# Optimization experiments

Measured on AMD Instinct MI355X. Metric: run time of the kernel, lower is better.

The kernel has to match this reference:

```python
import jax, jax.numpy as jnp
import numpy as np


def setup_inputs() -> dict:
    key = jax.random.key(0)
    k1, k2, k3, k4, k5 = jax.random.split(key, 5)
    B, TQ, TK, DQ, DV, U = 4, 512, 512, 512, 512, 256
    query = jax.random.normal(k1, (B, TQ, DQ), dtype=jnp.float32)
    value = jax.random.normal(k2, (B, TK, DV), dtype=jnp.float32)
    W1 = jax.random.normal(k3, (DQ, U), dtype=jnp.float32) * (1.0 / np.sqrt(DQ))
    W2 = jax.random.normal(k4, (DV, U), dtype=jnp.float32) * (1.0 / np.sqrt(DV))
    scale = jax.random.normal(k5, (U,), dtype=jnp.float32)
    return {"query": query, "value": value, "W1": W1, "W2": W2, "scale": scale}


def reference(query, value, W1, W2, scale):
    # Dense projections (no bias)
    q = jnp.einsum('bqd,du->bqu', query, W1)   # [B, Tq, U]
    k = jnp.einsum('bkd,du->bku', value, W2)   # [B, Tk, U]
    # Keras AdditiveAttention (use_scale=True):
    # scores[b,q,k] = sum_u scale[u] * tanh(q[b,q,u] + k[b,k,u])
    t = jnp.tanh(q[:, :, None, :] + k[:, None, :, :])  # [B, Tq, Tk, U]
    scores = jnp.einsum('bqku,u->bqk', t, scale)        # [B, Tq, Tk]
    attention_weights = jax.nn.softmax(scores, axis=-1)
    return attention_weights
```

## Files before the change

kernel.cpp:

```cpp
#include <hip/hip_runtime.h>

#define BB 4
#define TQ 512
#define TK 512
#define DQ 512
#define UU 256
#define CSC 2.8853900817779268f
#define L2E 1.4426950408889634f
#define RQ 4

typedef unsigned short u16;
typedef unsigned int u32;
typedef short bf16x8 __attribute__((ext_vector_type(8)));
typedef float f32x4 __attribute__((ext_vector_type(4)));

__device__ __forceinline__ float fexp2(float x) { return __builtin_amdgcn_exp2f(x); }
__device__ __forceinline__ float frcp(float x)  { return __builtin_amdgcn_rcpf(x); }
__device__ __forceinline__ u32 pkhi(u32 a, u32 b) { return (b & 0xffff0000u) | (a >> 16); }

__global__ __launch_bounds__(256) void wsplit(
    const float* __restrict__ W1, const float* __restrict__ W2,
    u16* __restrict__ W1h, u16* __restrict__ W1l,
    u16* __restrict__ W2h, u16* __restrict__ W2l)
{
    __shared__ float tile[32][33];
    const int blk = blockIdx.x, t = threadIdx.x;
    const float* W = (blk >> 7) ? W2 : W1;
    u16* oh = (blk >> 7) ? W2h : W1h;
    u16* ol = (blk >> 7) ? W2l : W1l;
    const int tl = blk & 127;
    const int k0 = (tl >> 3) * 32, n0 = (tl & 7) * 32;
    const int kl = t >> 5, nl = t & 31;
    #pragma unroll
    for (int r = 0; r < 4; r++)
        tile[kl + 8 * r][nl] = W[(size_t)(k0 + kl + 8 * r) * UU + n0 + nl];
    __syncthreads();
    const int nr = t >> 5, kc = t & 31;
    #pragma unroll
    for (int r = 0; r < 4; r++) {
        const float v = tile[kc][nr + 8 * r];
        const u32 x = __float_as_uint(v);
        const u16 h = (u16)(x >> 16);
        const u16 l = (u16)(__float_as_uint(v - __uint_as_float(x & 0xffff0000u)) >> 16);
        oh[(size_t)(n0 + nr + 8 * r) * DQ + k0 + kc] = h;
        ol[(size_t)(n0 + nr + 8 * r) * DQ + k0 + kc] = l;
    }
}

__global__ __launch_bounds__(256) void proj3(
    const float* __restrict__ Aq, const float* __restrict__ Av,
    const u16* __restrict__ W1h, const u16* __restrict__ W1l,
    const u16* __restrict__ W2h, const u16* __restrict__ W2l,
    float* __restrict__ Eq, float* __restrict__ Ek)
{
    __shared__ __align__(16) char raw[10240];
    float* fin = (float*)raw;

    const int z = blockIdx.z;
    const float* A = z ? Av : Aq;
    const u16* Wh = z ? W2h : W1h;
    const u16* Wl = z ? W2l : W1l;

    const int t = threadIdx.x;
    const int m0 = blockIdx.x * 32, n0 = blockIdx.y * 64;
    const int wave = t >> 6, ln = t & 15, qd = (t & 63) >> 4;
    const int arow = t >> 3, ak4 = (t & 7) * 4;
    const int ncol = n0 + wave * 16 + ln;
    const u16* whp = Wh + (size_t)ncol * DQ + qd * 8;
    const u16* wlp = Wl + (size_t)ncol * DQ + qd * 8;

    f32x4 acc[2] = {};

    float4 a4 = *(const float4*)&A[(size_t)(m0 + arow) * DQ + ak4];
    bf16x8 whc = *(const bf16x8*)&whp[0];
    bf16x8 wlc = *(const bf16x8*)&wlp[0];

    for (int i = 0; i < DQ / 32; i++) {
        char* buf = raw + (i & 1) * 5120;
        u16* Ah_s = (u16*)buf;
        u16* Al_s = (u16*)(buf + 2560);
        {
            const float f[4] = {a4.x, a4.y, a4.z, a4.w};
            u32 x[4], lx[4];
            #pragma unroll
            for (int e = 0; e < 4; e++) {
                x[e]  = __float_as_uint(f[e]);
                lx[e] = __float_as_uint(f[e] - __uint_as_float(x[e] & 0xffff0000u));
            }
            uint2 hw, lw;
            hw.x = pkhi(x[0], x[1]);  hw.y = pkhi(x[2], x[3]);
            lw.x = pkhi(lx[0], lx[1]); lw.y = pkhi(lx[2], lx[3]);
            *(uint2*)&Ah_s[arow * 40 + ak4] = hw;
            *(uint2*)&Al_s[arow * 40 + ak4] = lw;
        }
        if (i + 1 < DQ / 32)
            a4 = *(const float4*)&A[(size_t)(m0 + arow) * DQ + (i + 1) * 32 + ak4];
        __syncthreads();

        bf16x8 whn, wln;
        if (i + 1 < DQ / 32) {
            whn = *(const bf16x8*)&whp[(i + 1) * 32];
            wln = *(const bf16x8*)&wlp[(i + 1) * 32];
        }

        bf16x8 ah[2], al[2];
        #pragma unroll
        for (int ii = 0; ii < 2; ii++) {
            const int ar = (ii * 16 + ln) * 40 + qd * 8;
            ah[ii] = *(const bf16x8*)&Ah_s[ar];
            al[ii] = *(const bf16x8*)&Al_s[ar];
        }
        #pragma unroll
        for (int ii = 0; ii < 2; ii++) {
            acc[ii] = __builtin_amdgcn_mfma_f32_16x16x32_bf16(ah[ii], whc, acc[ii], 0, 0, 0);
            acc[ii] = __builtin_amdgcn_mfma_f32_16x16x32_bf16(ah[ii], wlc, acc[ii], 0, 0, 0);
            acc[ii] = __builtin_amdgcn_mfma_f32_16x16x32_bf16(al[ii], whc, acc[ii], 0, 0, 0);
        }
        whc = whn; wlc = wln;
    }

    if (z == 0) {
        #pragma unroll
        for (int ii = 0; ii < 2; ii++) {
            #pragma unroll
            for (int r = 0; r < 4; r++) {
                const int m = m0 + ii * 16 + qd * 4 + r;
                Eq[(size_t)m * UU + ncol] = fexp2(CSC * acc[ii][r]);
            }
        }
    } else {
        __syncthreads();
        #pragma unroll
        for (int ii = 0; ii < 2; ii++) {
            #pragma unroll
            for (int r = 0; r < 4; r++) {
                const int ml = ii * 16 + qd * 4 + r;
                const int nl = wave * 16 + ln;
                fin[ml * 68 + nl] = fexp2(CSC * acc[ii][r]);
            }
        }
        __syncthreads();
        const int b = m0 >> 9, j0 = m0 & 511;
        #pragma unroll
        for (int p = 0; p < 2; p++) {
            const int idx = p * 256 + t;
            const int jl = idx & 31, u4 = idx >> 5;
            const float4 v = *(const float4*)&fin[jl * 68 + u4 * 4];
            ((float4*)Ek)[(size_t)(b * (UU / 4) + (n0 >> 2) + u4) * TK + j0 + jl] = v;
        }
    }
}

__global__ __launch_bounds__(512) void attn_softmax(
    const float* __restrict__ Eq,
    const float* __restrict__ Ek,
    const float* __restrict__ scale,
    float* __restrict__ out)
{
    __shared__ float redbuf[RQ][8];
    const int t  = threadIdx.x;
    const int b  = blockIdx.x >> 7;
    const int q0 = (blockIdx.x & 127) * RQ;
    const float*  qrow = Eq + (size_t)(b * TQ + q0) * UU;
    const float4* kb4  = (const float4*)Ek + (size_t)b * (UU / 4) * TK + t;

    float acc[RQ] = {};

    auto body = [&](const float4& kv, int g) {
        const float4 sc4 = *(const float4*)&scale[4 * g];
        const float* sf = (const float*)&sc4;
        const float* kf = (const float*)&kv;
        #pragma unroll
        for (int r = 0; r < RQ; r++) {
            const float4 q4 = *(const float4*)&qrow[(size_t)r * UU + 4 * g];
            const float* qf = (const float*)&q4;
            #pragma unroll
            for (int p = 0; p < 4; p += 2) {
                const float d0 = fmaf(qf[p],     kf[p],     1.0f);
                const float d1 = fmaf(qf[p + 1], kf[p + 1], 1.0f);
                const float num = fmaf(sf[p], d1, sf[p + 1] * d0);
                acc[r] = fmaf(num, frcp(d0 * d1), acc[r]);
            }
        }
    };

    float4 c0 = kb4[0];
    float4 c1 = kb4[(size_t)TK];
    float4 c2 = kb4[(size_t)2 * TK];
    float4 c3 = kb4[(size_t)3 * TK];
    for (int g = 0; g < UU / 4; g += 4) {
        float4 n0v, n1v, n2v, n3v;
        if (g + 4 < UU / 4) {
            n0v = kb4[(size_t)(g + 4) * TK];
            n1v = kb4[(size_t)(g + 5) * TK];
            n2v = kb4[(size_t)(g + 6) * TK];
            n3v = kb4[(size_t)(g + 7) * TK];
        }
        body(c0, g); body(c1, g + 1); body(c2, g + 2); body(c3, g + 3);
        c0 = n0v; c1 = n1v; c2 = n2v; c3 = n3v;
    }
    #pragma unroll
    for (int r = 0; r < RQ; r++) acc[r] *= -2.0f;

    const int wave = t >> 6, lane = t & 63;
    float m[RQ], p[RQ];

    #pragma unroll
    for (int r = 0; r < RQ; r++) {
        float v = acc[r];
        #pragma unroll
        for (int o = 32; o > 0; o >>= 1) v = fmaxf(v, __shfl_xor(v, o));
        if (lane == 0) redbuf[r][wave] = v;
    }
    __syncthreads();
    #pragma unroll
    for (int r = 0; r < RQ; r++) {
        float v = redbuf[r][0];
        #pragma unroll
        for (int w = 1; w < 8; w++) v = fmaxf(v, redbuf[r][w]);
        m[r] = v;
    }
    __syncthreads();

    #pragma unroll
    for (int r = 0; r < RQ; r++) {
        p[r] = fexp2(L2E * (acc[r] - m[r]));
        float v = p[r];
        #pragma unroll
        for (int o = 32; o > 0; o >>= 1) v += __shfl_xor(v, o);
        if (lane == 0) redbuf[r][wave] = v;
    }
    __syncthreads();
    #pragma unroll
    for (int r = 0; r < RQ; r++) {
        float v = 0.0f;
        #pragma unroll
        for (int w = 0; w < 8; w++) v += redbuf[r][w];
        const float rinv = frcp(v);
        out[(size_t)(b * TQ + q0 + r) * TK + t] = p[r] * rinv;
    }
}

extern "C" void kernel_launch(void* const* d_in, const int* in_sizes, int n_in,
                              void* d_out, int out_size, void* d_ws, size_t ws_size,
                              hipStream_t stream) {
    const float* query = (const float*)d_in[0];
    const float* value = (const float*)d_in[1];
    const float* W1    = (const float*)d_in[2];
    const float* W2    = (const float*)d_in[3];
    const float* scale = (const float*)d_in[4];
    float* out = (float*)d_out;

    float* Eq = (float*)d_ws;
    float* Ek = Eq + (size_t)BB * TQ * UU;
    char* wbase = (char*)d_ws + 4 * 1048576;
    u16* W1h = (u16*)(wbase);
    u16* W1l = (u16*)(wbase + 262144);
    u16* W2h = (u16*)(wbase + 524288);
    u16* W2l = (u16*)(wbase + 786432);
    (void)ws_size;

    wsplit<<<256, 256, 0, stream>>>(W1, W2, W1h, W1l, W2h, W2l);
    proj3<<<dim3(64, 4, 2), 256, 0, stream>>>(query, value, W1h, W1l, W2h, W2l, Eq, Ek);
    attn_softmax<<<dim3(BB * TQ / RQ), 512, 0, stream>>>(Eq, Ek, scale, out);
}
```

Baseline: 108.2 us.

## Interleave Eq query rows in pairs and use packed-f32 math with one reciprocal per four units

```diff
diff --git a/kernel.cpp b/kernel.cpp
--- a/kernel.cpp
+++ b/kernel.cpp
@@ -13,6 +13,7 @@
 typedef unsigned int u32;
 typedef short bf16x8 __attribute__((ext_vector_type(8)));
 typedef float f32x4 __attribute__((ext_vector_type(4)));
+typedef float f32x2 __attribute__((ext_vector_type(2)));
 
 __device__ __forceinline__ float fexp2(float x) { return __builtin_amdgcn_exp2f(x); }
 __device__ __forceinline__ float frcp(float x)  { return __builtin_amdgcn_rcpf(x); }
@@ -123,9 +124,12 @@
         #pragma unroll
         for (int ii = 0; ii < 2; ii++) {
             #pragma unroll
-            for (int r = 0; r < 4; r++) {
+            for (int r = 0; r < 4; r += 2) {
                 const int m = m0 + ii * 16 + qd * 4 + r;
-                Eq[(size_t)m * UU + ncol] = fexp2(CSC * acc[ii][r]);
+                float2 v;
+                v.x = fexp2(CSC * acc[ii][r]);
+                v.y = fexp2(CSC * acc[ii][r + 1]);
+                *(float2*)&Eq[((size_t)(m >> 1) * UU + ncol) * 2] = v;
             }
         }
     } else {
@@ -164,23 +168,29 @@
     const float*  qrow = Eq + (size_t)(b * TQ + q0) * UU;
     const float4* kb4  = (const float4*)Ek + (size_t)b * (UU / 4) * TK + t;
 
-    float acc[RQ] = {};
+    f32x2 acc2[RQ / 2] = {};
 
     auto body = [&](const float4& kv, int g) {
         const float4 sc4 = *(const float4*)&scale[4 * g];
-        const float* sf = (const float*)&sc4;
-        const float* kf = (const float*)&kv;
-        #pragma unroll
-        for (int r = 0; r < RQ; r++) {
-            const float4 q4 = *(const float4*)&qrow[(size_t)r * UU + 4 * g];
-            const float* qf = (const float*)&q4;
-            #pragma unroll
-            for (int p = 0; p < 4; p += 2) {
-                const float d0 = fmaf(qf[p],     kf[p],     1.0f);
-                const float d1 = fmaf(qf[p + 1], kf[p + 1], 1.0f);
-                const float num = fmaf(sf[p], d1, sf[p + 1] * d0);
-                acc[r] = fmaf(num, frcp(d0 * d1), acc[r]);
-            }
+        const float s0 = sc4.x, s1 = sc4.y, s2 = sc4.z, s3 = sc4.w;
+        const float k0 = kv.x, k1 = kv.y, k2 = kv.z, k3 = kv.w;
+        #pragma unroll
+        for (int h = 0; h < RQ / 2; h++) {
+            const float4 qa = *(const float4*)&qrow[(size_t)h * (2 * UU) + 8 * g];
+            const float4 qb = *(const float4*)&qrow[(size_t)h * (2 * UU) + 8 * g + 4];
+            const f32x2 q0v = {qa.x, qa.y}, q1v = {qa.z, qa.w};
+            const f32x2 q2v = {qb.x, qb.y}, q3v = {qb.z, qb.w};
+            const f32x2 d0 = q0v * k0 + 1.0f;
+            const f32x2 d1 = q1v * k1 + 1.0f;
+            const f32x2 d2 = q2v * k2 + 1.0f;
+            const f32x2 d3 = q3v * k3 + 1.0f;
+            const f32x2 p01 = d0 * d1, p23 = d2 * d3;
+            const f32x2 n01 = s0 * d1 + s1 * d0;
+            const f32x2 n23 = s2 * d3 + s3 * d2;
+            const f32x2 num = n01 * p23 + n23 * p01;
+            const f32x2 den = p01 * p23;
+            const f32x2 rcp2 = {frcp(den.x), frcp(den.y)};
+            acc2[h] += num * rcp2;
         }
     };
 
@@ -199,15 +209,18 @@
         body(c0, g); body(c1, g + 1); body(c2, g + 2); body(c3, g + 3);
         c0 = n0v; c1 = n1v; c2 = n2v; c3 = n3v;
     }
-    #pragma unroll
-    for (int r = 0; r < RQ; r++) acc[r] *= -2.0f;
+
+    float accs[RQ];
+    #pragma unroll
+    for (int r = 0; r < RQ; r++)
+        accs[r] = ((r & 1) ? acc2[r >> 1].y : acc2[r >> 1].x) * -2.0f;
 
     const int wave = t >> 6, lane = t & 63;
     float m[RQ], p[RQ];
 
     #pragma unroll
     for (int r = 0; r < RQ; r++) {
-        float v = acc[r];
+        float v = accs[r];
         #pragma unroll
         for (int o = 32; o > 0; o >>= 1) v = fmaxf(v, __shfl_xor(v, o));
         if (lane == 0) redbuf[r][wave] = v;
@@ -224,7 +237,7 @@
 
     #pragma unroll
     for (int r = 0; r < RQ; r++) {
-        p[r] = fexp2(L2E * (acc[r] - m[r]));
+        p[r] = fexp2(L2E * (accs[r] - m[r]));
         float v = p[r];
         #pragma unroll
         for (int o = 32; o > 0; o >>= 1) v += __shfl_xor(v, o);
```

Result: slower. 111.6 us (+3.2%).
